# Performance work log

Hardware: AMD Instinct MI355X
Metric: run time of the kernel (lower is better)

## Reference

```python
import jax, jax.numpy as jnp
import numpy as np

N_NODES = 100000
N_EDGES = 1600000
D_IN = 128
D_HID = 128
N_CLASSES = 10
N_GRAPHS = 512


def setup_inputs() -> dict:
    key = jax.random.key(0)
    ks = jax.random.split(key, 12)
    x = jax.random.normal(ks[0], (N_NODES, D_IN), dtype=jnp.float32)
    edge_src = jax.random.randint(ks[1], (N_EDGES,), 0, N_NODES, dtype=jnp.int32)
    edge_dst = jax.random.randint(ks[2], (N_EDGES,), 0, N_NODES, dtype=jnp.int32)
    batch = jnp.sort(jax.random.randint(ks[3], (N_NODES,), 0, N_GRAPHS, dtype=jnp.int32))
    # GCNConv weights (glorot-ish scale) and biases
    def w(k, fi, fo):
        return jax.random.normal(k, (fi, fo), dtype=jnp.float32) / np.sqrt(fi)
    W0 = w(ks[4], D_IN, D_HID);  b0 = jnp.zeros((D_HID,), jnp.float32)
    W1 = w(ks[5], D_HID, D_HID); b1 = jnp.zeros((D_HID,), jnp.float32)
    W2 = w(ks[6], D_HID, D_HID); b2 = jnp.zeros((D_HID,), jnp.float32)
    Wc = w(ks[7], D_HID, N_CLASSES); bc = jnp.zeros((N_CLASSES,), jnp.float32)
    return {"x": x, "edge_src": edge_src, "edge_dst": edge_dst, "batch": batch,
            "W0": W0, "b0": b0, "W1": W1, "b1": b1, "W2": W2, "b2": b2,
            "Wc": Wc, "bc": bc}


def _gcn_conv(x, W, b, src, dst, dinv):
    # PyG GCNConv: h = x @ W; out[i] = sum_{j->i} dinv[j]*dinv[i]*h[j] (incl. self-loop) + b
    h = x @ W                                   # [N, F_out]
    norm = (dinv[src] * dinv[dst])[:, None]     # [E, 1]
    agg = jax.ops.segment_sum(h[src] * norm, dst, num_segments=N_NODES)
    agg = agg + h * (dinv * dinv)[:, None]      # self-loop contribution
    return agg + b


def reference(x, edge_src, edge_dst, batch, W0, b0, W1, b1, W2, b2, Wc, bc):
    # symmetric normalization: deg over dst with self-loops added
    deg = jax.ops.segment_sum(jnp.ones((N_EDGES,), jnp.float32), edge_dst,
                              num_segments=N_NODES) + 1.0
    dinv = jax.lax.rsqrt(deg)
    h = jax.nn.relu(_gcn_conv(x, W0, b0, edge_src, edge_dst, dinv))
    h = jax.nn.relu(_gcn_conv(h, W1, b1, edge_src, edge_dst, dinv))
    h = jax.nn.relu(_gcn_conv(h, W2, b2, edge_src, edge_dst, dinv))
    # global mean pool over graphs
    sums = jax.ops.segment_sum(h, batch, num_segments=N_GRAPHS)      # [G, D]
    cnts = jax.ops.segment_sum(jnp.ones((N_NODES,), jnp.float32), batch,
                               num_segments=N_GRAPHS)
    pooled = sums / jnp.maximum(cnts, 1.0)[:, None]
    return pooled @ Wc + bc                                          # [G, C]
```

## Files before the change

kernel.cpp:

```cpp
#include <hip/hip_runtime.h>

#define NN 100000
#define NE 1600000
#define DF 128
#define NG 512
#define NC 10
#define NBK 256
#define NPBN 391
#define BKCAP 8192
#define PCH 4096

typedef unsigned short u16;
typedef unsigned int u32;
typedef __bf16 bf16_t;
typedef bf16_t bf16x8 __attribute__((ext_vector_type(8)));
typedef float f32x4 __attribute__((ext_vector_type(4)));

__device__ __forceinline__ u16 f2bf(float f){
  u32 x=__float_as_uint(f);
  u32 r=(x+0x7fffu+((x>>16)&1u))>>16;
  return (u16)r;
}
__device__ __forceinline__ float bflo(u32 u){ return __uint_as_float(u<<16); }
__device__ __forceinline__ float bfhi(u32 u){ return __uint_as_float(u&0xffff0000u); }

__global__ void k_setup(int* __restrict__ cur,
                        const float* __restrict__ W0, const float* __restrict__ W1,
                        const float* __restrict__ W2, u16* __restrict__ WT,
                        const int* __restrict__ batch, int* __restrict__ goff){
  int i=blockIdx.x*256+threadIdx.x;
  if(i<NBK) cur[i]=0;
  if(i<3*DF*DF){
    int w=i>>14, r=i&16383;
    const float* W = (w==0)?W0:((w==1)?W1:W2);
    int k=r>>7, n=r&127;
    WT[(size_t)w*DF*DF + n*128+k]=f2bf(W[r]);
  }
  if(i<=NG){
    int lo=0, hi=NN;
    while(lo<hi){ int mid=(lo+hi)>>1; if(batch[mid]<i) lo=mid+1; else hi=mid; }
    goff[i]=lo;
  }
}

__global__ __launch_bounds__(256) void k_part(const int* __restrict__ esrc, const int* __restrict__ edst,
                                              int* __restrict__ cur, uint2* __restrict__ pairs, int n){
  __shared__ int hist[NBK], basev[NBK], lscan[NBK], lcur[NBK];
  __shared__ uint2 stage[PCH];
  int tid=threadIdx.x;
  int start=blockIdx.x*PCH, end=min(start+PCH,n);
  if(tid<NBK) hist[tid]=0;
  __syncthreads();
  for(int i=start+tid;i<end;i+=256) atomicAdd(&hist[(u32)edst[i]/NPBN],1);
  __syncthreads();
  if(tid<64){
    int carry=0;
    #pragma unroll
    for(int c=0;c<NBK;c+=64){
      int v=hist[c+tid], x=v;
      #pragma unroll
      for(int off=1;off<64;off<<=1){ int t=__shfl_up(x,off,64); if(tid>=off) x+=t; }
      lscan[c+tid]=x-v+carry;
      carry+=__shfl(x,63,64);
    }
  }
  __syncthreads();
  if(tid<NBK){ basev[tid]=atomicAdd(&cur[tid],hist[tid]); lcur[tid]=0; }
  __syncthreads();
  for(int i=start+tid;i<end;i+=256){
    int d=edst[i], s=esrc[i];
    int b=(u32)d/NPBN;
    int p=lscan[b]+atomicAdd(&lcur[b],1);
    stage[p]=make_uint2((u32)s,(u32)d);
  }
  __syncthreads();
  int ntot=end-start;
  for(int i=tid;i<ntot;i+=256){
    uint2 e=stage[i];
    int b=(u32)e.y/NPBN;
    pairs[(size_t)b*BKCAP + basev[b] + (i - lscan[b])]=e;
  }
}

__global__ __launch_bounds__(256) void k_bucket(const uint2* __restrict__ pairs, const int* __restrict__ cur,
                                                int* __restrict__ offs, float* __restrict__ dinv,
                                                int* __restrict__ csr){
  __shared__ int hist[NPBN], lsc[NPBN], curL[NBK];
  __shared__ int sbase[2];
  int b=blockIdx.x, tid=threadIdx.x;
  if(tid<NBK) curL[tid]=cur[tid];
  for(int j=tid;j<NPBN;j+=256) hist[j]=0;
  __syncthreads();
  if(tid<64){
    int acc=0;
    #pragma unroll
    for(int c=0;c<NBK;c+=64){
      int v=(c+tid<b)? curL[c+tid] : 0;
      #pragma unroll
      for(int off=32;off;off>>=1) v+=__shfl_xor(v,off,64);
      acc+=v;
    }
    if(tid==0){ sbase[0]=acc; sbase[1]=curL[b]; }
  }
  __syncthreads();
  int base=sbase[0], count=sbase[1];
  int node0=b*NPBN;
  int nnode=min(NPBN, NN-node0);
  const uint2* P=pairs+(size_t)b*BKCAP;
  for(int i=tid;i<count;i+=256) atomicAdd(&hist[P[i].y-node0],1);
  __syncthreads();
  if(tid<64){
    int carry=0;
    #pragma unroll
    for(int c=0;c<448;c+=64){
      int idx=c+tid;
      int v=(idx<NPBN)? hist[idx] : 0, x=v;
      #pragma unroll
      for(int off=1;off<64;off<<=1){ int t=__shfl_up(x,off,64); if(tid>=off) x+=t; }
      if(idx<NPBN) lsc[idx]=x-v+carry;
      carry+=__shfl(x,63,64);
    }
  }
  __syncthreads();
  for(int j=tid;j<nnode;j+=256){
    offs[node0+j]=base+lsc[j];
    dinv[node0+j]=rsqrtf((float)hist[j]+1.0f);
  }
  if(b==NBK-1 && tid==0) offs[NN]=base+count;
  __syncthreads();
  for(int j=tid;j<nnode;j+=256) hist[j]=lsc[j];
  __syncthreads();
  for(int i=tid;i<count;i+=256){
    uint2 e=P[i];
    int p=atomicAdd(&hist[e.y-node0],1);
    csr[base+p]=(int)e.x;
  }
}

template<bool F32IN>
__global__ __launch_bounds__(256) void k_gemm(const void* __restrict__ Ap, const u16* __restrict__ WT,
                                              const float* __restrict__ dinv, u16* __restrict__ outp, int n){
  __shared__ u16 sA[128][136];
  __shared__ u16 sW[128][136];
  int tid=threadIdx.x;
  int row0=blockIdx.x*128;
  {
    const uint4* p=(const uint4*)WT;
    #pragma unroll
    for(int j=0;j<8;++j){
      int c=tid+j*256;
      int r=c>>4, c8=c&15;
      *(uint4*)&sW[r][c8*8]=p[c];
    }
  }
  if(F32IN){
    const float4* A4=(const float4*)Ap;
    #pragma unroll
    for(int j=0;j<16;++j){
      int c=tid+j*256;
      int r=c>>5, c4=c&31;
      int row=row0+r;
      float4 v = (row<n)? A4[(size_t)row*32+c4] : make_float4(0.f,0.f,0.f,0.f);
      u32 lo=(u32)f2bf(v.x) | ((u32)f2bf(v.y)<<16);
      u32 hi=(u32)f2bf(v.z) | ((u32)f2bf(v.w)<<16);
      uint2 q; q.x=lo; q.y=hi;
      *(uint2*)&sA[r][c4*4]=q;
    }
  } else {
    const uint4* A4=(const uint4*)Ap;
    #pragma unroll
    for(int j=0;j<8;++j){
      int c=tid+j*256;
      int r=c>>4, c8=c&15;
      int row=row0+r;
      uint4 v = (row<n)? A4[(size_t)row*16+c8] : make_uint4(0,0,0,0);
      *(uint4*)&sA[r][c8*8]=v;
    }
  }
  __syncthreads();
  int wv=tid>>6, lane=tid&63;
  int lr=lane&15, lk=lane>>4;
  f32x4 acc[2][8];
  #pragma unroll
  for(int mr=0;mr<2;++mr)
    #pragma unroll
    for(int nt=0;nt<8;++nt) acc[mr][nt]=(f32x4){0.f,0.f,0.f,0.f};
  #pragma unroll
  for(int kk=0;kk<4;++kk){
    bf16x8 a[2], b[8];
    #pragma unroll
    for(int mr=0;mr<2;++mr)
      a[mr]=*(const bf16x8*)&sA[wv*32+mr*16+lr][kk*32+lk*8];
    #pragma unroll
    for(int nt=0;nt<8;++nt)
      b[nt]=*(const bf16x8*)&sW[nt*16+lr][kk*32+lk*8];
    #pragma unroll
    for(int mr=0;mr<2;++mr)
      #pragma unroll
      for(int nt=0;nt<8;++nt)
        acc[mr][nt]=__builtin_amdgcn_mfma_f32_16x16x32_bf16(a[mr],b[nt],acc[mr][nt],0,0,0);
  }
  #pragma unroll
  for(int mr=0;mr<2;++mr){
    int rbase=row0+wv*32+mr*16+lk*4;
    #pragma unroll
    for(int r=0;r<4;++r){
      int row=rbase+r;
      if(row<n){
        float di=dinv[row];
        #pragma unroll
        for(int nt=0;nt<8;++nt)
          outp[(size_t)row*128+nt*16+lr]=f2bf(acc[mr][nt][r]*di);
      }
    }
  }
}

__global__ __launch_bounds__(256) void k_agg(const u16* __restrict__ h2, const int* __restrict__ offs,
                                             const int* __restrict__ csr, const float* __restrict__ dinv,
                                             const float* __restrict__ bias, u16* __restrict__ outp, int n){
  int wid=threadIdx.x>>6, lane=threadIdx.x&63;
  int node=blockIdx.x*4+wid;
  if(node>=n) return;
  const u32* hv=(const u32*)h2;
  u32 sv=hv[(size_t)node*64+lane];
  float ax=bflo(sv), ay=bfhi(sv);
  int e=offs[node], e1=offs[node+1];
  for(; e+16<=e1; e+=16){
    int ii[16];
    #pragma unroll
    for(int j=0;j<16;++j) ii[j]=csr[e+j];
    u32 vv[16];
    #pragma unroll
    for(int j=0;j<16;++j) vv[j]=hv[(size_t)ii[j]*64+lane];
    #pragma unroll
    for(int j=0;j<16;++j){ ax+=bflo(vv[j]); ay+=bfhi(vv[j]); }
  }
  if(e+8<=e1){
    int ii[8];
    #pragma unroll
    for(int j=0;j<8;++j) ii[j]=csr[e+j];
    u32 vv[8];
    #pragma unroll
    for(int j=0;j<8;++j) vv[j]=hv[(size_t)ii[j]*64+lane];
    #pragma unroll
    for(int j=0;j<8;++j){ ax+=bflo(vv[j]); ay+=bfhi(vv[j]); }
    e+=8;
  }
  if(e+4<=e1){
    int i0=csr[e],i1=csr[e+1],i2=csr[e+2],i3=csr[e+3];
    u32 v0=hv[(size_t)i0*64+lane], v1=hv[(size_t)i1*64+lane];
    u32 v2=hv[(size_t)i2*64+lane], v3=hv[(size_t)i3*64+lane];
    ax+=bflo(v0)+bflo(v1)+bflo(v2)+bflo(v3);
    ay+=bfhi(v0)+bfhi(v1)+bfhi(v2)+bfhi(v3);
    e+=4;
  }
  if(e+2<=e1){
    int i0=csr[e],i1=csr[e+1];
    u32 v0=hv[(size_t)i0*64+lane], v1=hv[(size_t)i1*64+lane];
    ax+=bflo(v0)+bflo(v1);
    ay+=bfhi(v0)+bfhi(v1);
    e+=2;
  }
  if(e<e1){
    u32 v=hv[(size_t)csr[e]*64+lane];
    ax+=bflo(v); ay+=bfhi(v);
  }
  float di=dinv[node];
  float2 b=*(const float2*)&bias[lane*2];
  float ox=fmaf(di,ax,b.x), oy=fmaf(di,ay,b.y);
  ox=ox>0.f?ox:0.f; oy=oy>0.f?oy:0.f;
  u32 o=(u32)f2bf(ox) | ((u32)f2bf(oy)<<16);
  ((u32*)outp)[(size_t)node*64+lane]=o;
}

__global__ __launch_bounds__(512) void k_pool(const u16* __restrict__ h, const int* __restrict__ goff,
                                              const float* __restrict__ Wc, const float* __restrict__ bc,
                                              float* __restrict__ outp){
  __shared__ float part[8][128];
  __shared__ float pooled[128];
  int g=blockIdx.x;
  int tid=threadIdx.x, wid=tid>>6, lane=tid&63;
  int i0=goff[g], i1=goff[g+1];
  const u32* hv=(const u32*)h;
  float ax=0.f, ay=0.f;
  for(int i=i0+wid;i<i1;i+=8){
    u32 v=hv[(size_t)i*64+lane];
    ax+=bflo(v); ay+=bfhi(v);
  }
  part[wid][lane*2]=ax; part[wid][lane*2+1]=ay;
  __syncthreads();
  if(tid<128){
    float s=part[0][tid]+part[1][tid]+part[2][tid]+part[3][tid]
           +part[4][tid]+part[5][tid]+part[6][tid]+part[7][tid];
    int cnt=i1-i0;
    pooled[tid]=(cnt>0)? s/(float)cnt : 0.f;
  }
  __syncthreads();
  if(tid<NC){
    float s=bc[tid];
    #pragma unroll 16
    for(int k=0;k<128;++k) s=fmaf(pooled[k], Wc[k*NC+tid], s);
    outp[g*NC+tid]=s;
  }
}

extern "C" void kernel_launch(void* const* d_in, const int* in_sizes, int n_in,
                              void* d_out, int out_size, void* d_ws, size_t ws_size,
                              hipStream_t stream){
  const float* x   =(const float*)d_in[0];
  const int* esrc  =(const int*)d_in[1];
  const int* edst  =(const int*)d_in[2];
  const int* batch =(const int*)d_in[3];
  const float* W0=(const float*)d_in[4];
  const float* b0=(const float*)d_in[5];
  const float* W1=(const float*)d_in[6];
  const float* b1=(const float*)d_in[7];
  const float* W2=(const float*)d_in[8];
  const float* b2=(const float*)d_in[9];
  const float* Wc=(const float*)d_in[10];
  const float* bc=(const float*)d_in[11];
  float* out=(float*)d_out;

  char* base=(char*)d_ws; size_t off=0;
  auto alloc=[&](size_t bytes)->void*{ off=(off+255)&~(size_t)255; void* p=base+off; off+=bytes; return p; };
  int*   cur  =(int*)  alloc(NBK*4);
  int*   offs =(int*)  alloc((size_t)(NN+1)*4);
  int*   goff =(int*)  alloc((NG+1)*4);
  float* dinv =(float*)alloc((size_t)NN*4);
  int*   csr  =(int*)  alloc((size_t)NE*4);
  uint2* pairs=(uint2*)alloc((size_t)NBK*BKCAP*8);
  u16*   WT   =(u16*)  alloc((size_t)3*DF*DF*2);
  u16*   bufA =(u16*)  alloc((size_t)NN*DF*2);
  u16*   bufB =(u16*)  alloc((size_t)NN*DF*2);
  (void)ws_size; (void)in_sizes; (void)n_in; (void)out_size;

  hipLaunchKernelGGL(k_setup,  dim3(192),  dim3(256), 0, stream, cur, W0, W1, W2, WT, batch, goff);
  hipLaunchKernelGGL(k_part,   dim3((NE+PCH-1)/PCH), dim3(256), 0, stream, esrc, edst, cur, pairs, NE);
  hipLaunchKernelGGL(k_bucket, dim3(NBK),  dim3(256), 0, stream, pairs, cur, offs, dinv, csr);

  const int GB=(NN+127)/128;
  const int AB=(NN+3)/4;

  k_gemm<true ><<<dim3(GB), dim3(256), 0, stream>>>((const void*)x,    WT,           dinv, bufA, NN);
  hipLaunchKernelGGL(k_agg,  dim3(AB), dim3(256), 0, stream, bufA, offs, csr, dinv, b0, bufB, NN);
  k_gemm<false><<<dim3(GB), dim3(256), 0, stream>>>((const void*)bufB, WT+DF*DF,     dinv, bufA, NN);
  hipLaunchKernelGGL(k_agg,  dim3(AB), dim3(256), 0, stream, bufA, offs, csr, dinv, b1, bufB, NN);
  k_gemm<false><<<dim3(GB), dim3(256), 0, stream>>>((const void*)bufB, WT+2*DF*DF,   dinv, bufA, NN);
  hipLaunchKernelGGL(k_agg,  dim3(AB), dim3(256), 0, stream, bufA, offs, csr, dinv, b2, bufB, NN);
  hipLaunchKernelGGL(k_pool, dim3(NG), dim3(512), 0, stream, bufB, goff, Wc, bc, out);
}
```

Baseline: 306.9 us.

## Fuse aggregation with the following layer's GEMM in one kernel

Adds a k_fuse kernel in which each 512-thread block aggregates 128 nodes (16 per wavefront) into shared memory, then multiplies that tile by the next layer's weights with MFMA. This replaces the agg→gemm kernel pairs for layers 0→1 and 1→2. The aim is to avoid writing and re-reading the intermediate activations and to save launches. In exchange, each block carries a serial gather phase of 16 nodes per wave before any MFMA work, and it uses a large shared-memory footprint that may lower occupancy and latency hiding for the gathers.

```diff
diff --git a/kernel.cpp b/kernel.cpp
--- a/kernel.cpp
+++ b/kernel.cpp
@@ -23,6 +23,50 @@
 }
 __device__ __forceinline__ float bflo(u32 u){ return __uint_as_float(u<<16); }
 __device__ __forceinline__ float bfhi(u32 u){ return __uint_as_float(u&0xffff0000u); }
+
+__device__ __forceinline__ void agg_node(const u32* __restrict__ hv, const int* __restrict__ csr,
+                                         int e, int e1, int lane, float& ax, float& ay){
+  for(; e+16<=e1; e+=16){
+    int ii[16];
+    #pragma unroll
+    for(int j=0;j<16;++j) ii[j]=csr[e+j];
+    u32 vv[16];
+    #pragma unroll
+    for(int j=0;j<16;++j) vv[j]=hv[(size_t)ii[j]*64+lane];
+    #pragma unroll
+    for(int j=0;j<16;++j){ ax+=bflo(vv[j]); ay+=bfhi(vv[j]); }
+  }
+  if(e+8<=e1){
+    int ii[8];
+    #pragma unroll
+    for(int j=0;j<8;++j) ii[j]=csr[e+j];
+    u32 vv[8];
+    #pragma unroll
+    for(int j=0;j<8;++j) vv[j]=hv[(size_t)ii[j]*64+lane];
+    #pragma unroll
+    for(int j=0;j<8;++j){ ax+=bflo(vv[j]); ay+=bfhi(vv[j]); }
+    e+=8;
+  }
+  if(e+4<=e1){
+    int i0=csr[e],i1=csr[e+1],i2=csr[e+2],i3=csr[e+3];
+    u32 v0=hv[(size_t)i0*64+lane], v1=hv[(size_t)i1*64+lane];
+    u32 v2=hv[(size_t)i2*64+lane], v3=hv[(size_t)i3*64+lane];
+    ax+=bflo(v0)+bflo(v1)+bflo(v2)+bflo(v3);
+    ay+=bfhi(v0)+bfhi(v1)+bfhi(v2)+bfhi(v3);
+    e+=4;
+  }
+  if(e+2<=e1){
+    int i0=csr[e],i1=csr[e+1];
+    u32 v0=hv[(size_t)i0*64+lane], v1=hv[(size_t)i1*64+lane];
+    ax+=bflo(v0)+bflo(v1);
+    ay+=bfhi(v0)+bfhi(v1);
+    e+=2;
+  }
+  if(e<e1){
+    u32 v=hv[(size_t)csr[e]*64+lane];
+    ax+=bflo(v); ay+=bfhi(v);
+  }
+}
 
 __global__ void k_setup(int* __restrict__ cur,
                         const float* __restrict__ W0, const float* __restrict__ W1,
@@ -137,9 +181,8 @@
   }
 }
 
-template<bool F32IN>
-__global__ __launch_bounds__(256) void k_gemm(const void* __restrict__ Ap, const u16* __restrict__ WT,
-                                              const float* __restrict__ dinv, u16* __restrict__ outp, int n){
+__global__ __launch_bounds__(256) void k_gemm0(const float* __restrict__ A, const u16* __restrict__ WT,
+                                               const float* __restrict__ dinv, u16* __restrict__ outp, int n){
   __shared__ u16 sA[128][136];
   __shared__ u16 sW[128][136];
   int tid=threadIdx.x;
@@ -153,8 +196,8 @@
       *(uint4*)&sW[r][c8*8]=p[c];
     }
   }
-  if(F32IN){
-    const float4* A4=(const float4*)Ap;
+  {
+    const float4* A4=(const float4*)A;
     #pragma unroll
     for(int j=0;j<16;++j){
       int c=tid+j*256;
@@ -166,16 +209,6 @@
       uint2 q; q.x=lo; q.y=hi;
       *(uint2*)&sA[r][c4*4]=q;
     }
-  } else {
-    const uint4* A4=(const uint4*)Ap;
-    #pragma unroll
-    for(int j=0;j<8;++j){
-      int c=tid+j*256;
-      int r=c>>4, c8=c&15;
-      int row=row0+r;
-      uint4 v = (row<n)? A4[(size_t)row*16+c8] : make_uint4(0,0,0,0);
-      *(uint4*)&sA[r][c8*8]=v;
-    }
   }
   __syncthreads();
   int wv=tid>>6, lane=tid&63;
@@ -212,6 +245,70 @@
         for(int nt=0;nt<8;++nt)
           outp[(size_t)row*128+nt*16+lr]=f2bf(acc[mr][nt][r]*di);
       }
+    }
+  }
+}
+
+__global__ __launch_bounds__(512) void k_fuse(const u16* __restrict__ h2in, const int* __restrict__ offs,
+                                              const int* __restrict__ csr, const float* __restrict__ dinv,
+                                              const float* __restrict__ biasv, const u16* __restrict__ WT,
+                                              u16* __restrict__ outp, int n){
+  __shared__ u16 sA[128][136];
+  __shared__ u16 sW[128][136];
+  int tid=threadIdx.x;
+  int row0=blockIdx.x*128;
+  {
+    const uint4* p=(const uint4*)WT;
+    #pragma unroll
+    for(int j=0;j<4;++j){
+      int c=tid+j*512;
+      int r=c>>4, c8=c&15;
+      *(uint4*)&sW[r][c8*8]=p[c];
+    }
+  }
+  int wid=tid>>6, lane=tid&63;
+  const u32* hv=(const u32*)h2in;
+  float2 bv=*(const float2*)&biasv[lane*2];
+  for(int k=0;k<16;++k){
+    int local=wid*16+k;
+    int node=row0+local;
+    u32 oword=0;
+    if(node<n){
+      u32 sv=hv[(size_t)node*64+lane];
+      float ax=bflo(sv), ay=bfhi(sv);
+      agg_node(hv, csr, offs[node], offs[node+1], lane, ax, ay);
+      float di=dinv[node];
+      float ox=fmaf(di,ax,bv.x), oy=fmaf(di,ay,bv.y);
+      ox=ox>0.f?ox:0.f; oy=oy>0.f?oy:0.f;
+      oword=(u32)f2bf(ox) | ((u32)f2bf(oy)<<16);
+    }
+    *(u32*)&sA[local][lane*2]=oword;
+  }
+  __syncthreads();
+  int lr=lane&15, lk=lane>>4;
+  f32x4 acc[8];
+  #pragma unroll
+  for(int nt=0;nt<8;++nt) acc[nt]=(f32x4){0.f,0.f,0.f,0.f};
+  #pragma unroll
+  for(int kk=0;kk<4;++kk){
+    bf16x8 a=*(const bf16x8*)&sA[wid*16+lr][kk*32+lk*8];
+    bf16x8 b[8];
+    #pragma unroll
+    for(int nt=0;nt<8;++nt)
+      b[nt]=*(const bf16x8*)&sW[nt*16+lr][kk*32+lk*8];
+    #pragma unroll
+    for(int nt=0;nt<8;++nt)
+      acc[nt]=__builtin_amdgcn_mfma_f32_16x16x32_bf16(a,b[nt],acc[nt],0,0,0);
+  }
+  int rbase=row0+wid*16+lk*4;
+  #pragma unroll
+  for(int r=0;r<4;++r){
+    int row=rbase+r;
+    if(row<n){
+      float di=dinv[row];
+      #pragma unroll
+      for(int nt=0;nt<8;++nt)
+        outp[(size_t)row*128+nt*16+lr]=f2bf(acc[nt][r]*di);
     }
   }
 }
@@ -225,47 +322,7 @@
   const u32* hv=(const u32*)h2;
   u32 sv=hv[(size_t)node*64+lane];
   float ax=bflo(sv), ay=bfhi(sv);
-  int e=offs[node], e1=offs[node+1];
-  for(; e+16<=e1; e+=16){
-    int ii[16];
-    #pragma unroll
-    for(int j=0;j<16;++j) ii[j]=csr[e+j];
-    u32 vv[16];
-    #pragma unroll
-    for(int j=0;j<16;++j) vv[j]=hv[(size_t)ii[j]*64+lane];
-    #pragma unroll
-    for(int j=0;j<16;++j){ ax+=bflo(vv[j]); ay+=bfhi(vv[j]); }
-  }
-  if(e+8<=e1){
-    int ii[8];
-    #pragma unroll
-    for(int j=0;j<8;++j) ii[j]=csr[e+j];
-    u32 vv[8];
-    #pragma unroll
-    for(int j=0;j<8;++j) vv[j]=hv[(size_t)ii[j]*64+lane];
-    #pragma unroll
-    for(int j=0;j<8;++j){ ax+=bflo(vv[j]); ay+=bfhi(vv[j]); }
-    e+=8;
-  }
-  if(e+4<=e1){
-    int i0=csr[e],i1=csr[e+1],i2=csr[e+2],i3=csr[e+3];
-    u32 v0=hv[(size_t)i0*64+lane], v1=hv[(size_t)i1*64+lane];
-    u32 v2=hv[(size_t)i2*64+lane], v3=hv[(size_t)i3*64+lane];
-    ax+=bflo(v0)+bflo(v1)+bflo(v2)+bflo(v3);
-    ay+=bfhi(v0)+bfhi(v1)+bfhi(v2)+bfhi(v3);
-    e+=4;
-  }
-  if(e+2<=e1){
-    int i0=csr[e],i1=csr[e+1];
-    u32 v0=hv[(size_t)i0*64+lane], v1=hv[(size_t)i1*64+lane];
-    ax+=bflo(v0)+bflo(v1);
-    ay+=bfhi(v0)+bfhi(v1);
-    e+=2;
-  }
-  if(e<e1){
-    u32 v=hv[(size_t)csr[e]*64+lane];
-    ax+=bflo(v); ay+=bfhi(v);
-  }
+  agg_node(hv, csr, offs[node], offs[node+1], lane, ax, ay);
   float di=dinv[node];
   float2 b=*(const float2*)&bias[lane*2];
   float ox=fmaf(di,ax,b.x), oy=fmaf(di,ay,b.y);
@@ -342,11 +399,9 @@
   const int GB=(NN+127)/128;
   const int AB=(NN+3)/4;
 
-  k_gemm<true ><<<dim3(GB), dim3(256), 0, stream>>>((const void*)x,    WT,           dinv, bufA, NN);
-  hipLaunchKernelGGL(k_agg,  dim3(AB), dim3(256), 0, stream, bufA, offs, csr, dinv, b0, bufB, NN);
-  k_gemm<false><<<dim3(GB), dim3(256), 0, stream>>>((const void*)bufB, WT+DF*DF,     dinv, bufA, NN);
-  hipLaunchKernelGGL(k_agg,  dim3(AB), dim3(256), 0, stream, bufA, offs, csr, dinv, b1, bufB, NN);
-  k_gemm<false><<<dim3(GB), dim3(256), 0, stream>>>((const void*)bufB, WT+2*DF*DF,   dinv, bufA, NN);
-  hipLaunchKernelGGL(k_agg,  dim3(AB), dim3(256), 0, stream, bufA, offs, csr, dinv, b2, bufB, NN);
-  hipLaunchKernelGGL(k_pool, dim3(NG), dim3(512), 0, stream, bufB, goff, Wc, bc, out);
-}
+  hipLaunchKernelGGL(k_gemm0, dim3(GB), dim3(256), 0, stream, x, WT, dinv, bufA, NN);
+  hipLaunchKernelGGL(k_fuse,  dim3(GB), dim3(512), 0, stream, bufA, offs, csr, dinv, b0, WT+DF*DF,   bufB, NN);
+  hipLaunchKernelGGL(k_fuse,  dim3(GB), dim3(512), 0, stream, bufB, offs, csr, dinv, b1, WT+2*DF*DF, bufA, NN);
+  hipLaunchKernelGGL(k_agg,   dim3(AB), dim3(256), 0, stream, bufA, offs, csr, dinv, b2, bufB, NN);
+  hipLaunchKernelGGL(k_pool,  dim3(NG), dim3(512), 0, stream, bufB, goff, Wc, bc, out);
+}
```

Result: slower. 349.3 us (+13.8%).
